# Optimization experiments

Hardware: AMD Instinct MI355X
Metric: run time of the kernel (lower is better)

Reference implementation:

```python
import jax, jax.numpy as jnp
import numpy as np

B, N, IN, OUT, H = 8, 256, 256, 256, 4
HD = OUT // H  # 64
ALPHA = 0.2    # LeakyReLU negative slope
EPS = 1e-5


def layernorm(x, g, b):
    m = x.mean(-1, keepdims=True)
    v = jnp.mean(jnp.square(x - m), axis=-1, keepdims=True)
    return (x - m) / jnp.sqrt(v + EPS) * g + b


def setup_inputs() -> dict:
    key = jax.random.key(0)
    ks = jax.random.split(key, 16)
    s = 0.05
    return {
        'h':    jax.random.normal(ks[0], (B, N, IN), jnp.float32),
        'adj':  jax.random.randint(ks[1], (B, N, N), 0, 2, jnp.int32),
        # per-head params (leading dim H)
        'W':    jax.random.normal(ks[2], (H, IN, HD), jnp.float32) * s,      # node proj (no bias)
        'We1':  jax.random.normal(ks[3], (H, 2 * IN, HD), jnp.float32) * s,  # edge_encoder lin
        'be1':  jnp.zeros((H, HD), jnp.float32),
        'Wa1':  jax.random.normal(ks[4], (H, 3 * HD, HD), jnp.float32) * s,  # attn mlp lin1
        'ba1':  jnp.zeros((H, HD), jnp.float32),
        'wa2':  jax.random.normal(ks[5], (H, HD), jnp.float32) * s,          # attn mlp lin2 -> scalar
        'ba2':  jnp.zeros((H,), jnp.float32),
        'ln_g': jnp.ones((H, HD), jnp.float32),   # per-head LayerNorm
        'ln_b': jnp.zeros((H, HD), jnp.float32),
        'Wo':   jax.random.normal(ks[6], (OUT, OUT), jnp.float32) * s,       # output projection
        'bo':   jnp.zeros((OUT,), jnp.float32),
        'ln2_g': jnp.ones((OUT,), jnp.float32),   # final LayerNorm
        'ln2_b': jnp.zeros((OUT,), jnp.float32),
    }


def _head(h, adj_mask, W, We1, be1, Wa1, ba1, wa2, ba2, g, b):
    # h: [B,N,IN]; adj_mask: [B,N,N] bool (True where adj==0)
    Wh = jnp.einsum('bnf,fd->bnd', h, W)                      # [B,N,HD]
    # attention MLP lin1 applied to concat([Wh_i, Wh_j, edge]):
    # split weight so the per-node parts are computed once, broadcast over pairs
    Wa, Wb, We = Wa1[:HD], Wa1[HD:2 * HD], Wa1[2 * HD:]
    si = jnp.einsum('bnd,de->bne', Wh, Wa) + ba1              # [B,N,HD]
    sj = jnp.einsum('bnd,de->bne', Wh, Wb)                    # [B,N,HD]
    # edge encoder: Linear(cat[h_i,h_j]) -> leaky_relu, split likewise
    ei = jnp.einsum('bnf,fd->bnd', h, We1[:IN]) + be1         # [B,N,HD]
    ej = jnp.einsum('bnf,fd->bnd', h, We1[IN:])               # [B,N,HD]
    edge = jax.nn.leaky_relu(ei[:, :, None, :] + ej[:, None, :, :], ALPHA)  # [B,N,N,HD]
    hidden = jax.nn.leaky_relu(
        si[:, :, None, :] + sj[:, None, :, :] + jnp.einsum('bijd,de->bije', edge, We),
        ALPHA)                                                # [B,N,N,HD]
    e = jnp.einsum('bijd,d->bij', hidden, wa2) + ba2          # [B,N,N]
    e = jnp.where(adj_mask, -1e9, e)
    attn = jax.nn.softmax(e, axis=-1)                         # [B,N,N]
    hp = jnp.einsum('bij,bjd->bid', attn, Wh)                 # [B,N,HD]
    return layernorm(hp, g, b)


def reference(h, adj, W, We1, be1, Wa1, ba1, wa2, ba2, ln_g, ln_b, Wo, bo, ln2_g, ln2_b):
    adj_mask = (adj == 0)
    heads = [
        _head(h, adj_mask, W[i], We1[i], be1[i], Wa1[i], ba1[i],
              wa2[i], ba2[i], ln_g[i], ln_b[i])
        for i in range(H)
    ]
    concat = jnp.concatenate(heads, axis=-1)                  # [B,N,OUT]
    out = jnp.einsum('bnf,fo->bno', concat, Wo) + bo
    out = out + h                                             # residual (IN == OUT)
    return layernorm(out, ln2_g, ln2_b)
```

## Files before the change

### kernel.cpp

```cpp
#include <hip/hip_runtime.h>
#include <hip/hip_bf16.h>

#define B_ 8
#define N_ 256
#define IN_ 256
#define OUT_ 256
#define H_ 4
#define HD_ 64
#define ALPHA_ 0.2f
#define EPS_ 1e-5f

#define S_ (B_*H_*N_*HD_)


typedef unsigned short ushort_t;
typedef __attribute__((ext_vector_type(8))) short short8;
typedef __attribute__((ext_vector_type(4))) float floatx4;

__device__ __forceinline__ float lrelu(float x) { return fmaxf(x, ALPHA_ * x); }
__device__ __forceinline__ ushort_t f2b(float x) {
    unsigned u = __float_as_uint(x);
    unsigned r = ((u >> 16) & 1u) + 0x7fffu;
    return (ushort_t)((u + r) >> 16);
}
__device__ __forceinline__ unsigned pk2(float x0, float x1) {
    __hip_bfloat162 p = __float22bfloat162_rn(make_float2(x0, x1));
    return *(unsigned*)&p;
}
template<int STRIDE>
__device__ __forceinline__ short8 gcol(const float* __restrict__ base) {
    union { unsigned u[4]; short8 s; } w;
    #pragma unroll
    for (int p = 0; p < 4; ++p)
        w.u[p] = pk2(base[(2 * p) * STRIDE], base[(2 * p + 1) * STRIDE]);
    return w.s;
}

__global__ __launch_bounds__(256) void prep2_kernel(
    const float* __restrict__ h, const float* __restrict__ W,
    const float* __restrict__ We1, const float* __restrict__ be1,
    float* __restrict__ ws)
{
    const int gm = blockIdx.x & 127, gn = blockIdx.x >> 7;
    const int tid = threadIdx.x, lane = tid & 63, wid = tid >> 6;
    const int quad = lane >> 4, l15 = lane & 15;

    float*    ei_f = ws;
    ushort_t* ej_b = (ushort_t*)(ws + S_);
    ushort_t* Wh_b = ej_b + S_;

    int headA[2], typeA[2], dA[2];
    const float* wbase[2];
    #pragma unroll
    for (int nt = 0; nt < 2; ++nt) {
        const int colg = gn * 128 + wid * 32 + nt * 16 + l15;
        const int head = colg / 192;
        const int c    = colg - head * 192;
        const int type = c >> 6, d = c & 63;
        headA[nt] = head; typeA[nt] = type; dA[nt] = d;
        if (type == 0)      wbase[nt] = W   + (size_t)head * 16384 + d;
        else if (type == 1) wbase[nt] = We1 + (size_t)head * 32768 + d;
        else                wbase[nt] = We1 + (size_t)head * 32768 + 16384 + d;
    }

    floatx4 acc[2];
    #pragma unroll
    for (int nt = 0; nt < 2; ++nt) acc[nt] = (floatx4){0.f,0.f,0.f,0.f};

    #pragma unroll 2
    for (int ks = 0; ks < 8; ++ks) {
        const float* hp0 = &h[(size_t)(gm * 16 + l15) * 256 + ks * 32 + quad * 8];
        float4 a0 = *(const float4*)hp0;
        float4 a1 = *(const float4*)(hp0 + 4);
        union { unsigned u[4]; short8 s; } aw;
        aw.u[0] = pk2(a0.x, a0.y); aw.u[1] = pk2(a0.z, a0.w);
        aw.u[2] = pk2(a1.x, a1.y); aw.u[3] = pk2(a1.z, a1.w);
        #pragma unroll
        for (int nt = 0; nt < 2; ++nt) {
            short8 bfr = gcol<64>(wbase[nt] + (size_t)(ks * 32 + quad * 8) * 64);
            acc[nt] = __builtin_amdgcn_mfma_f32_16x16x32_bf16(aw.s, bfr, acc[nt], 0, 0, 0);
        }
    }

    #pragma unroll
    for (int nt = 0; nt < 2; ++nt) {
        const int head = headA[nt], type = typeA[nt], d = dA[nt];
        #pragma unroll
        for (int reg = 0; reg < 4; ++reg) {
            const int row = gm * 16 + quad * 4 + reg;
            const int b = row >> 8, n = row & 255;
            const size_t idx = ((size_t)(b * H_ + head) * 256 + n) * 64 + d;
            const float v = acc[nt][reg];
            if      (type == 0) Wh_b[idx] = f2b(v);
            else if (type == 1) ei_f[idx] = v + be1[head * 64 + d];
            else                ej_b[idx] = f2b(v);
        }
    }
}

__global__ __launch_bounds__(256, 2) void attn_kernel(
    const int* __restrict__ adj, const float* __restrict__ Wa1,
    const float* __restrict__ ba1, const float* __restrict__ wa2,
    const float* __restrict__ ba2, const float* __restrict__ ln_g,
    const float* __restrict__ ln_b, float* __restrict__ ws)
{
    const int blk  = blockIdx.x;
    const int ig   = blk & 15;
    const int head = (blk >> 4) & 3;
    const int b    = blk >> 6;
    const int i0   = ig * 16;
    const int tid  = threadIdx.x;
    const int lane = tid & 63;
    const int wid  = tid >> 6;
    const int quad = lane >> 4;
    const int l15  = lane & 15;
    const int bh   = b * H_ + head;

    __shared__ float    P_s[16 * 256];
    __shared__ ushort_t Pb_s[16 * 264];
    __shared__ float    ei_s[16 * 64];
    __shared__ float    si_s[16 * 64];
    __shared__ unsigned long long adjm_s[16 * 4];
    __shared__ float    hp_s[16 * 68];

    const float*    ei_f = ws;
    const ushort_t* ej_b = (const ushort_t*)(ws + S_);
    const ushort_t* Wh_b = ej_b + S_;
    ushort_t*       conc = (ushort_t*)(ws + 2 * (size_t)S_);
    const float*    wa_base = Wa1 + (size_t)head * 12288;

    {
        const int ii = tid >> 4, c = tid & 15;
        *(float4*)&ei_s[ii * 64 + c * 4] =
            *(const float4*)&ei_f[((size_t)(bh * 256 + i0 + ii)) * 64 + c * 4];
    }
    {
        int av[16];
        #pragma unroll
        for (int r = 0; r < 16; ++r)
            av[r] = adj[((size_t)(b * 256 + i0 + r)) * 256 + tid];
        #pragma unroll
        for (int r = 0; r < 16; ++r) {
            unsigned long long mk = __ballot(av[r] != 0);
            if (lane == 0) adjm_s[r * 4 + wid] = mk;
        }
    }

    uint4   ejr[4][2];
    short8  afrWe[4][2];
    floatx4 sjaccT[4][4];
    float   w6[4][4], w4[4][4];
    #pragma unroll
    for (int nt = 0; nt < 4; ++nt) {
        const size_t jrow = (size_t)(bh * 256 + wid * 64 + nt * 16 + l15) * 64;
        #pragma unroll
        for (int kk = 0; kk < 2; ++kk)
            ejr[nt][kk] = *(const uint4*)&ej_b[jrow + kk * 32 + quad * 8];
    }
    #pragma unroll
    for (int mt = 0; mt < 4; ++mt) {
        #pragma unroll
        for (int ks = 0; ks < 2; ++ks)
            afrWe[mt][ks] = gcol<64>(wa_base + (size_t)(128 + ks * 32 + quad * 8) * 64
                                     + mt * 16 + l15);
        float4 wvv = *(const float4*)&wa2[head * 64 + mt * 16 + quad * 4];
        w6[mt][0] = 0.6f * wvv.x; w4[mt][0] = 0.4f * wvv.x;
        w6[mt][1] = 0.6f * wvv.y; w4[mt][1] = 0.4f * wvv.y;
        w6[mt][2] = 0.6f * wvv.z; w4[mt][2] = 0.4f * wvv.z;
        w6[mt][3] = 0.6f * wvv.w; w4[mt][3] = 0.4f * wvv.w;
    }
    {
        #pragma unroll
        for (int mt = 0; mt < 4; ++mt)
            #pragma unroll
            for (int nt = 0; nt < 4; ++nt) sjaccT[mt][nt] = (floatx4){0.f,0.f,0.f,0.f};
        #pragma unroll
        for (int ks = 2; ks < 4; ++ks) {
            short8 aWb[4], bWh[4];
            #pragma unroll
            for (int mt = 0; mt < 4; ++mt)
                aWb[mt] = gcol<64>(wa_base + (size_t)(64 + (ks - 2) * 32 + quad * 8) * 64
                                   + mt * 16 + l15);
            #pragma unroll
            for (int nt = 0; nt < 4; ++nt)
                bWh[nt] = *(const short8*)&Wh_b[((size_t)(bh * 256 + wid * 64 + nt * 16 + l15)) * 64
                                                + (ks - 2) * 32 + quad * 8];
            #pragma unroll
            for (int mt = 0; mt < 4; ++mt)
                #pragma unroll
                for (int nt = 0; nt < 4; ++nt)
                    sjaccT[mt][nt] = __builtin_amdgcn_mfma_f32_16x16x32_bf16(
                        aWb[mt], bWh[nt], sjaccT[mt][nt], 0, 0, 0);
        }
    }
    {
        floatx4 siacc = (floatx4){0.f,0.f,0.f,0.f};
        #pragma unroll
        for (int ks = 0; ks < 2; ++ks) {
            short8 aWh = *(const short8*)&Wh_b[((size_t)(bh * 256 + i0 + l15)) * 64
                                               + ks * 32 + quad * 8];
            short8 bWa = gcol<64>(wa_base + (size_t)(ks * 32 + quad * 8) * 64
                                  + wid * 16 + l15);
            siacc = __builtin_amdgcn_mfma_f32_16x16x32_bf16(aWh, bWa, siacc, 0, 0, 0);
        }
        const float ba1v = ba1[head * 64 + wid * 16 + l15];
        #pragma unroll
        for (int reg = 0; reg < 4; ++reg)
            si_s[(quad * 4 + reg) * 64 + wid * 16 + l15] = siacc[reg] + ba1v;
    }
    const float ba2h = ba2[head];

    __syncthreads();

    for (int i = 0; i < 16; ++i) {
        floatx4 acc[4][4];
        #pragma unroll
        for (int ks = 0; ks < 2; ++ks) {
            short8 tfr[4];
            float ev[8];
            *(float4*)&ev[0] = *(const float4*)&ei_s[i * 64 + ks * 32 + quad * 8];
            *(float4*)&ev[4] = *(const float4*)&ei_s[i * 64 + ks * 32 + quad * 8 + 4];
            #pragma unroll
            for (int nt = 0; nt < 4; ++nt) {
                const unsigned* rw = (const unsigned*)&ejr[nt][ks];
                union { unsigned u[4]; short8 s; } ow;
                #pragma unroll
                for (int p = 0; p < 4; ++p) {
                    float x0 = __uint_as_float(rw[p] << 16)         + ev[2 * p];
                    float x1 = __uint_as_float(rw[p] & 0xffff0000u) + ev[2 * p + 1];
                    ow.u[p] = pk2(lrelu(x0), lrelu(x1));
                }
                tfr[nt] = ow.s;
            }
            if (ks == 0) {
                #pragma unroll
                for (int mt = 0; mt < 4; ++mt)
                    #pragma unroll
                    for (int nt = 0; nt < 4; ++nt)
                        acc[mt][nt] = __builtin_amdgcn_mfma_f32_16x16x32_bf16(
                            afrWe[mt][0], tfr[nt], sjaccT[mt][nt], 0, 0, 0);
            } else {
                #pragma unroll
                for (int mt = 0; mt < 4; ++mt)
                    #pragma unroll
                    for (int nt = 0; nt < 4; ++nt)
                        acc[mt][nt] = __builtin_amdgcn_mfma_f32_16x16x32_bf16(
                            afrWe[mt][1], tfr[nt], acc[mt][nt], 0, 0, 0);
            }
        }

        float sv[4][4];
        #pragma unroll
        for (int mt = 0; mt < 4; ++mt)
            *(float4*)&sv[mt][0] = *(const float4*)&si_s[i * 64 + mt * 16 + quad * 4];
        #pragma unroll
        for (int nt = 0; nt < 4; ++nt) {
            float val = 0.f;
            #pragma unroll
            for (int mt = 0; mt < 4; ++mt)
                #pragma unroll
                for (int reg = 0; reg < 4; ++reg) {
                    const float t = acc[mt][nt][reg] + sv[mt][reg];
                    val = fmaf(t, w6[mt][reg], val);
                    val = fmaf(fabsf(t), w4[mt][reg], val);
                }
            val += __shfl_xor(val, 16, 64);
            val += __shfl_xor(val, 32, 64);
            if (quad == 0)
                P_s[i * 256 + wid * 64 + nt * 16 + l15] = val + ba2h;
        }
    }
    __syncthreads();

    #pragma unroll
    for (int rr = 0; rr < 4; ++rr) {
        const int r = rr * 4 + wid;
        float4 v = *(const float4*)&P_s[r * 256 + lane * 4];
        const unsigned mk = (unsigned)(adjm_s[r * 4 + quad] >> (l15 * 4)) & 0xFu;
        float v0 = (mk & 1u) ? v.x : -1e9f;
        float v1 = (mk & 2u) ? v.y : -1e9f;
        float v2 = (mk & 4u) ? v.z : -1e9f;
        float v3 = (mk & 8u) ? v.w : -1e9f;
        float m = fmaxf(fmaxf(v0, v1), fmaxf(v2, v3));
        #pragma unroll
        for (int off = 32; off >= 1; off >>= 1) m = fmaxf(m, __shfl_xor(m, off, 64));
        float p0 = __expf(v0 - m), p1 = __expf(v1 - m);
        float p2 = __expf(v2 - m), p3 = __expf(v3 - m);
        float s = (p0 + p1) + (p2 + p3);
        #pragma unroll
        for (int off = 32; off >= 1; off >>= 1) s += __shfl_xor(s, off, 64);
        const float inv = 1.f / s;
        uint2 o; o.x = pk2(p0 * inv, p1 * inv); o.y = pk2(p2 * inv, p3 * inv);
        *(uint2*)&Pb_s[r * 264 + lane * 4] = o;
    }
    __syncthreads();

    floatx4 hacc = (floatx4){0.f,0.f,0.f,0.f};
    #pragma unroll
    for (int s = 0; s < 8; ++s) {
        short8 af = *(const short8*)&Pb_s[l15 * 264 + s * 32 + quad * 8];
        short8 bf;
        #pragma unroll
        for (int jj = 0; jj < 8; ++jj)
            bf[jj] = (short)Wh_b[((size_t)(bh * 256) + s * 32 + quad * 8 + jj) * 64 + wid * 16 + l15];
        hacc = __builtin_amdgcn_mfma_f32_16x16x32_bf16(af, bf, hacc, 0, 0, 0);
    }
    #pragma unroll
    for (int reg = 0; reg < 4; ++reg)
        hp_s[(quad * 4 + reg) * 68 + wid * 16 + l15] = hacc[reg];
    __syncthreads();

    const float gg = ln_g[head * 64 + lane];
    const float bb = ln_b[head * 64 + lane];
    #pragma unroll
    for (int pss = 0; pss < 4; ++pss) {
        const int r = pss * 4 + wid;
        const float v = hp_s[r * 68 + lane];
        float s1 = v, s2 = v * v;
        #pragma unroll
        for (int off = 32; off >= 1; off >>= 1) {
            s1 += __shfl_xor(s1, off, 64);
            s2 += __shfl_xor(s2, off, 64);
        }
        const float mean = s1 * (1.f / 64.f);
        const float var = s2 * (1.f / 64.f) - mean * mean;
        const float o = (v - mean) * __frsqrt_rn(var + EPS_) * gg + bb;
        conc[((size_t)(b * 256 + i0 + r)) * 256 + head * 64 + lane] = f2b(o);
    }
}

__global__ __launch_bounds__(256) void out2_kernel(
    const float* __restrict__ h, const float* __restrict__ Wo,
    const float* __restrict__ bo, const float* __restrict__ ln2_g,
    const float* __restrict__ ln2_b, const ushort_t* __restrict__ conc,
    float* __restrict__ out)
{
    const int rowbase = blockIdx.x * 8;
    const int tid = threadIdx.x, lane = tid & 63, wid = tid >> 6;
    const int quad = lane >> 4, l15 = lane & 15;

    __shared__ float s1a[8][4], s2a[8][4];

    floatx4 acc[4];
    #pragma unroll
    for (int nt = 0; nt < 4; ++nt) acc[nt] = (floatx4){0.f,0.f,0.f,0.f};

    #pragma unroll 2
    for (int ks = 0; ks < 8; ++ks) {
        short8 afr = *(const short8*)&conc[(size_t)(rowbase + (l15 & 7)) * 256 + ks * 32 + quad * 8];
        #pragma unroll
        for (int nt = 0; nt < 4; ++nt) {
            short8 bfr = gcol<256>(Wo + (size_t)(ks * 32 + quad * 8) * 256
                                   + wid * 64 + nt * 16 + l15);
            acc[nt] = __builtin_amdgcn_mfma_f32_16x16x32_bf16(afr, bfr, acc[nt], 0, 0, 0);
        }
    }

    float x[4][4];
    if (quad < 2) {
        float s1[4], s2[4];
        #pragma unroll
        for (int reg = 0; reg < 4; ++reg) { s1[reg] = 0.f; s2[reg] = 0.f; }
        #pragma unroll
        for (int nt = 0; nt < 4; ++nt) {
            const int col = wid * 64 + nt * 16 + l15;
            const float bv = bo[col];
            #pragma unroll
            for (int reg = 0; reg < 4; ++reg) {
                const int row = rowbase + quad * 4 + reg;
                float v = acc[nt][reg] + bv + h[(size_t)row * 256 + col];
                x[nt][reg] = v;
                s1[reg] += v;
                s2[reg] += v * v;
            }
        }
        #pragma unroll
        for (int reg = 0; reg < 4; ++reg) {
            #pragma unroll
            for (int off = 1; off <= 8; off <<= 1) {
                s1[reg] += __shfl_xor(s1[reg], off, 64);
                s2[reg] += __shfl_xor(s2[reg], off, 64);
            }
            if (l15 == 0) {
                s1a[quad * 4 + reg][wid] = s1[reg];
                s2a[quad * 4 + reg][wid] = s2[reg];
            }
        }
    }
    __syncthreads();

    if (quad < 2) {
        #pragma unroll
        for (int reg = 0; reg < 4; ++reg) {
            const int r = quad * 4 + reg;
            const float S1 = s1a[r][0] + s1a[r][1] + s1a[r][2] + s1a[r][3];
            const float S2 = s2a[r][0] + s2a[r][1] + s2a[r][2] + s2a[r][3];
            const float mean = S1 * (1.f / 256.f);
            const float var = S2 * (1.f / 256.f) - mean * mean;
            const float rs = __frsqrt_rn(var + EPS_);
            const int row = rowbase + r;
            #pragma unroll
            for (int nt = 0; nt < 4; ++nt) {
                const int col = wid * 64 + nt * 16 + l15;
                out[(size_t)row * 256 + col] =
                    (x[nt][reg] - mean) * rs * ln2_g[col] + ln2_b[col];
            }
        }
    }
}

extern "C" void kernel_launch(void* const* d_in, const int* in_sizes, int n_in,
                              void* d_out, int out_size, void* d_ws, size_t ws_size,
                              hipStream_t stream)
{
    const float* h    = (const float*)d_in[0];
    const int*   adj  = (const int*)  d_in[1];
    const float* W    = (const float*)d_in[2];
    const float* We1  = (const float*)d_in[3];
    const float* be1  = (const float*)d_in[4];
    const float* Wa1  = (const float*)d_in[5];
    const float* ba1  = (const float*)d_in[6];
    const float* wa2  = (const float*)d_in[7];
    const float* ba2  = (const float*)d_in[8];
    const float* ln_g = (const float*)d_in[9];
    const float* ln_b = (const float*)d_in[10];
    const float* Wo   = (const float*)d_in[11];
    const float* bo   = (const float*)d_in[12];
    const float* ln2g = (const float*)d_in[13];
    const float* ln2b = (const float*)d_in[14];

    float* ws = (float*)d_ws;
    ushort_t* conc = (ushort_t*)(ws + 2 * (size_t)S_);
    float* out = (float*)d_out;

    prep2_kernel<<<768, 256, 0, stream>>>(h, W, We1, be1, ws);
    attn_kernel <<<512, 256, 0, stream>>>(adj, Wa1, ba1, wa2, ba2, ln_g, ln_b, ws);
    out2_kernel <<<256, 256, 0, stream>>>(h, Wo, bo, ln2g, ln2b, conc, out);
}
```

Baseline: 155.3 us.

## Pre-transpose Wo to bf16 in prep kernel and halve out-kernel rows per block

Adds 16 extra blocks to the prep kernel that transpose Wo through shared memory and store it as bf16. The output kernel can then load B fragments with a single 16-byte vector load instead of eight strided fp32 gathers plus conversions. The output kernel also handles 4 rows per block instead of 8 and launches 512 blocks for more parallelism, though that leaves more lanes of each MFMA tile idle. The wider shared-memory tile declared in prep2 may lower occupancy for the main prep blocks.

```diff
diff --git a/kernel.cpp b/kernel.cpp
--- a/kernel.cpp
+++ b/kernel.cpp
@@ -39,10 +39,26 @@
 __global__ __launch_bounds__(256) void prep2_kernel(
     const float* __restrict__ h, const float* __restrict__ W,
     const float* __restrict__ We1, const float* __restrict__ be1,
+    const float* __restrict__ Wo, ushort_t* __restrict__ wo_t,
     float* __restrict__ ws)
 {
+    const int tid = threadIdx.x;
+    __shared__ float tl[64][65];
+
+    if (blockIdx.x >= 768) {
+        const int bb = blockIdx.x - 768;
+        const int to = bb & 3, tf = bb >> 2;
+        const int r4 = tid >> 6, cl = tid & 63;
+        for (int rr = r4; rr < 64; rr += 4)
+            tl[rr][cl] = Wo[(size_t)(tf * 64 + rr) * 256 + to * 64 + cl];
+        __syncthreads();
+        for (int rr = r4; rr < 64; rr += 4)
+            wo_t[(size_t)(to * 64 + rr) * 256 + tf * 64 + cl] = f2b(tl[cl][rr]);
+        return;
+    }
+
     const int gm = blockIdx.x & 127, gn = blockIdx.x >> 7;
-    const int tid = threadIdx.x, lane = tid & 63, wid = tid >> 6;
+    const int lane = tid & 63, wid = tid >> 6;
     const int quad = lane >> 4, l15 = lane & 15;
 
     float*    ei_f = ws;
@@ -330,16 +346,16 @@
 }
 
 __global__ __launch_bounds__(256) void out2_kernel(
-    const float* __restrict__ h, const float* __restrict__ Wo,
-    const float* __restrict__ bo, const float* __restrict__ ln2_g,
-    const float* __restrict__ ln2_b, const ushort_t* __restrict__ conc,
+    const float* __restrict__ h, const float* __restrict__ bo,
+    const float* __restrict__ ln2_g, const float* __restrict__ ln2_b,
+    const ushort_t* __restrict__ conc, const ushort_t* __restrict__ wo_t,
     float* __restrict__ out)
 {
-    const int rowbase = blockIdx.x * 8;
+    const int rowbase = blockIdx.x * 4;
     const int tid = threadIdx.x, lane = tid & 63, wid = tid >> 6;
     const int quad = lane >> 4, l15 = lane & 15;
 
-    __shared__ float s1a[8][4], s2a[8][4];
+    __shared__ float s1a[4][4], s2a[4][4];
 
     floatx4 acc[4];
     #pragma unroll
@@ -347,17 +363,16 @@
 
     #pragma unroll 2
     for (int ks = 0; ks < 8; ++ks) {
-        short8 afr = *(const short8*)&conc[(size_t)(rowbase + (l15 & 7)) * 256 + ks * 32 + quad * 8];
+        short8 afr = *(const short8*)&conc[(size_t)(rowbase + (l15 & 3)) * 256 + ks * 32 + quad * 8];
         #pragma unroll
         for (int nt = 0; nt < 4; ++nt) {
-            short8 bfr = gcol<256>(Wo + (size_t)(ks * 32 + quad * 8) * 256
-                                   + wid * 64 + nt * 16 + l15);
+            short8 bfr = *(const short8*)&wo_t[(size_t)(wid * 64 + nt * 16 + l15) * 256 + ks * 32 + quad * 8];
             acc[nt] = __builtin_amdgcn_mfma_f32_16x16x32_bf16(afr, bfr, acc[nt], 0, 0, 0);
         }
     }
 
     float x[4][4];
-    if (quad < 2) {
+    if (quad == 0) {
         float s1[4], s2[4];
         #pragma unroll
         for (int reg = 0; reg < 4; ++reg) { s1[reg] = 0.f; s2[reg] = 0.f; }
@@ -367,7 +382,7 @@
             const float bv = bo[col];
             #pragma unroll
             for (int reg = 0; reg < 4; ++reg) {
-                const int row = rowbase + quad * 4 + reg;
+                const int row = rowbase + reg;
                 float v = acc[nt][reg] + bv + h[(size_t)row * 256 + col];
                 x[nt][reg] = v;
                 s1[reg] += v;
@@ -382,23 +397,22 @@
                 s2[reg] += __shfl_xor(s2[reg], off, 64);
             }
             if (l15 == 0) {
-                s1a[quad * 4 + reg][wid] = s1[reg];
-                s2a[quad * 4 + reg][wid] = s2[reg];
+                s1a[reg][wid] = s1[reg];
+                s2a[reg][wid] = s2[reg];
             }
         }
     }
     __syncthreads();
 
-    if (quad < 2) {
+    if (quad == 0) {
         #pragma unroll
         for (int reg = 0; reg < 4; ++reg) {
-            const int r = quad * 4 + reg;
-            const float S1 = s1a[r][0] + s1a[r][1] + s1a[r][2] + s1a[r][3];
-            const float S2 = s2a[r][0] + s2a[r][1] + s2a[r][2] + s2a[r][3];
+            const float S1 = s1a[reg][0] + s1a[reg][1] + s1a[reg][2] + s1a[reg][3];
+            const float S2 = s2a[reg][0] + s2a[reg][1] + s2a[reg][2] + s2a[reg][3];
             const float mean = S1 * (1.f / 256.f);
             const float var = S2 * (1.f / 256.f) - mean * mean;
             const float rs = __frsqrt_rn(var + EPS_);
-            const int row = rowbase + r;
+            const int row = rowbase + reg;
             #pragma unroll
             for (int nt = 0; nt < 4; ++nt) {
                 const int col = wid * 64 + nt * 16 + l15;
@@ -431,9 +445,10 @@
 
     float* ws = (float*)d_ws;
     ushort_t* conc = (ushort_t*)(ws + 2 * (size_t)S_);
+    ushort_t* wo_t = conc + 524288;
     float* out = (float*)d_out;
 
-    prep2_kernel<<<768, 256, 0, stream>>>(h, W, We1, be1, ws);
+    prep2_kernel<<<784, 256, 0, stream>>>(h, W, We1, be1, Wo, wo_t, ws);
     attn_kernel <<<512, 256, 0, stream>>>(adj, Wa1, ba1, wa2, ba2, ln_g, ln_b, ws);
-    out2_kernel <<<256, 256, 0, stream>>>(h, Wo, bo, ln2g, ln2b, conc, out);
-}
+    out2_kernel <<<512, 256, 0, stream>>>(h, bo, ln2g, ln2b, conc, wo_t, out);
+}
```

Result: slower. 160.8 us (+3.5%).
